# Performance work log

Hardware: AMD Instinct MI355X
Metric: run time of the kernel (lower is better)

The kernel has to match this reference:

```python
import jax, jax.numpy as jnp
import numpy as np


def setup_inputs() -> dict:
    key = jax.random.key(0)
    ks = jax.random.split(key, 8)
    B, Te, De, Dd, H = 64, 1024, 1024, 1024, 1024
    return {
        "encoder_outputs": jax.random.normal(ks[0], (B, Te, De), jnp.float32),
        "decoder_outputs": jax.random.normal(ks[1], (B, 1, Dd), jnp.float32),
        "Wa_w": jax.random.normal(ks[2], (H, Dd), jnp.float32) * 0.02,
        "Wa_b": jax.random.normal(ks[3], (H,), jnp.float32) * 0.02,
        "Ua_w": jax.random.normal(ks[4], (H, De), jnp.float32) * 0.02,
        "Ua_b": jax.random.normal(ks[5], (H,), jnp.float32) * 0.02,
        "Va_w": jax.random.normal(ks[6], (1, H), jnp.float32) * 0.02,
        "Va_b": jax.random.normal(ks[7], (1,), jnp.float32) * 0.02,
    }


def reference(encoder_outputs, decoder_outputs, Wa_w, Wa_b, Ua_w, Ua_b, Va_w, Va_b):
    # Wa: [B,1,H], Ua: [B,Te,H]  (torch Linear: x @ W.T + b)
    Wa = jnp.einsum('bqd,hd->bqh', decoder_outputs, Wa_w) + Wa_b
    Ua = jnp.einsum('bed,hd->beh', encoder_outputs, Ua_w) + Ua_b
    # broadcast add -> tanh -> scalar score per encoder position: [B,Te,1]
    scores = jnp.einsum('beh,oh->beo', jnp.tanh(Wa + Ua), Va_w) + Va_b
    scores = jnp.transpose(scores, (0, 2, 1))          # [B,1,Te]
    weights = jax.nn.softmax(scores, axis=-1)          # softmax over Te
    context = jnp.einsum('bqe,bed->bqd', weights, encoder_outputs)  # [B,1,De]
    return context
```

## Files before the change

kernel.cpp:

```cpp
#include <hip/hip_runtime.h>
#include <hip/hip_bf16.h>

#define B_  64
#define TE  1024
#define K_  1024
#define HH  1024
#define MM  (B_ * TE)

typedef __bf16 bf16x8 __attribute__((ext_vector_type(8)));
typedef __bf16 bf16x4 __attribute__((ext_vector_type(4)));
typedef float  f32x4  __attribute__((ext_vector_type(4)));

__device__ __forceinline__ float fast_tanh(float x) {
    float ax = __builtin_fabsf(x);
    float t  = __expf(-2.0f * ax);
    float r  = (1.0f - t) * __builtin_amdgcn_rcpf(1.0f + t);
    return __builtin_copysignf(r, x);
}

__global__ void zero_kernel(float* __restrict__ a, float* __restrict__ b, int n) {
    int i = blockIdx.x * blockDim.x + threadIdx.x;
    if (i < n) { a[i] = 0.0f; b[i] = 0.0f; }
}

__global__ void cvt_kernel(const float* __restrict__ in, __bf16* __restrict__ out, long n4) {
    long i = (long)blockIdx.x * blockDim.x + threadIdx.x;
    long stride = (long)gridDim.x * blockDim.x;
    const float4* in4 = (const float4*)in;
    bf16x4* out4 = (bf16x4*)out;
    for (long j = i; j < n4; j += stride) {
        float4 v = in4[j];
        bf16x4 o;
        o[0] = (__bf16)v.x; o[1] = (__bf16)v.y; o[2] = (__bf16)v.z; o[3] = (__bf16)v.w;
        out4[j] = o;
    }
}

__global__ void wa_kernel(const float* __restrict__ dec, const float* __restrict__ Wa_w,
                          const float* __restrict__ Wa_b, float* __restrict__ WaOut) {
    int b = blockIdx.x, ht = blockIdx.y;
    int wave = threadIdx.x >> 6, lane = threadIdx.x & 63;
    const float* db = dec + b * 1024;
    for (int i = 0; i < 16; i++) {
        int h = ht * 64 + wave * 16 + i;
        const float* wr = Wa_w + (long)h * 1024;
        float a = 0.0f;
        #pragma unroll
        for (int k = 0; k < 16; k++)
            a += db[lane + 64 * k] * wr[lane + 64 * k];
        #pragma unroll
        for (int off = 32; off > 0; off >>= 1)
            a += __shfl_xor(a, off, 64);
        if (lane == 0) WaOut[b * 1024 + h] = a + Wa_b[h];
    }
}

#define MT 128
#define KT 64
#define NTILES 4

__global__ __launch_bounds__(256, 4) void score_gemm(
    const __bf16* __restrict__ A,
    const __bf16* __restrict__ Bm,
    const float* __restrict__ Wa,
    const float* __restrict__ Ua_b,
    const float* __restrict__ Va_w,
    float* __restrict__ scores)
{
    __shared__ __bf16 sA[MT * KT];
    __shared__ __bf16 sB[MT * KT];
    __shared__ float sVa[512];
    __shared__ float sWU[512];

    const int tid  = threadIdx.x;
    const int wave = tid >> 6;
    const int lane = tid & 63;
    const int quad = lane >> 4;
    const int l16  = lane & 15;
    const int wm   = wave >> 1;
    const int wn   = wave & 1;

    const int rowBase = blockIdx.x * MT;
    const int colBase = blockIdx.y * (NTILES * 128);
    const int b       = rowBase >> 10;

    for (int i = tid; i < 512; i += 256) {
        int h = colBase + i;
        sVa[i] = Va_w[h];
        sWU[i] = Wa[b * 1024 + h] + Ua_b[h];
    }

    float rs[4][4] = {};

    const long aBase = (long)rowBase * K_;
    for (int nt = 0; nt < NTILES; nt++) {
        f32x4 acc[4][4] = {};
        const long bBase = (long)(colBase + nt * 128) * K_;

        for (int k0 = 0; k0 < K_; k0 += KT) {
            __syncthreads();
            #pragma unroll
            for (int i = 0; i < 4; i++) {
                int c = i * 256 + tid;
                int r = c >> 3, slot = c & 7;
                int seg = slot ^ (r & 7);
                __builtin_amdgcn_global_load_lds(
                    (const __attribute__((address_space(1))) unsigned int*)(A + aBase + (long)r * K_ + k0 + seg * 8),
                    (__attribute__((address_space(3))) unsigned int*)(sA + c * 8), 16, 0, 0);
            }
            #pragma unroll
            for (int i = 0; i < 4; i++) {
                int c = i * 256 + tid;
                int r = c >> 3, slot = c & 7;
                int seg = slot ^ (r & 7);
                __builtin_amdgcn_global_load_lds(
                    (const __attribute__((address_space(1))) unsigned int*)(Bm + bBase + (long)r * K_ + k0 + seg * 8),
                    (__attribute__((address_space(3))) unsigned int*)(sB + c * 8), 16, 0, 0);
            }
            __syncthreads();

            #pragma unroll
            for (int ks = 0; ks < 2; ks++) {
                bf16x8 bfr[4];
                #pragma unroll
                for (int t = 0; t < 4; t++) {
                    int r = wn * 64 + t * 16 + l16;
                    int slot = (ks * 4 + quad) ^ (r & 7);
                    bfr[t] = *(const bf16x8*)(sB + r * KT + slot * 8);
                }
                #pragma unroll
                for (int s = 0; s < 4; s++) {
                    int r = wm * 64 + s * 16 + l16;
                    int slot = (ks * 4 + quad) ^ (r & 7);
                    bf16x8 af = *(const bf16x8*)(sA + r * KT + slot * 8);
                    #pragma unroll
                    for (int t = 0; t < 4; t++)
                        acc[s][t] = __builtin_amdgcn_mfma_f32_16x16x32_bf16(af, bfr[t], acc[s][t], 0, 0, 0);
                }
            }
        }

        #pragma unroll
        for (int s = 0; s < 4; s++)
            #pragma unroll
            for (int t = 0; t < 4; t++) {
                int hl = nt * 128 + wn * 64 + t * 16 + l16;
                float va = sVa[hl], wu = sWU[hl];
                #pragma unroll
                for (int r = 0; r < 4; r++)
                    rs[s][r] += va * fast_tanh(acc[s][t][r] + wu);
            }
    }

    #pragma unroll
    for (int s = 0; s < 4; s++)
        #pragma unroll
        for (int r = 0; r < 4; r++) {
            float v = rs[s][r];
            v += __shfl_xor(v, 1, 64);
            v += __shfl_xor(v, 2, 64);
            v += __shfl_xor(v, 4, 64);
            v += __shfl_xor(v, 8, 64);
            if (l16 == 0)
                atomicAdd(&scores[rowBase + wm * 64 + s * 16 + quad * 4 + r], v);
        }
}

__global__ void softmax_kernel(float* __restrict__ s) {
    __shared__ float red[256];
    int b = blockIdx.x, tid = threadIdx.x;
    float4* row = (float4*)(s + b * 1024);
    float4 v = row[tid];
    float m = fmaxf(fmaxf(v.x, v.y), fmaxf(v.z, v.w));
    red[tid] = m; __syncthreads();
    for (int off = 128; off > 0; off >>= 1) {
        if (tid < off) red[tid] = fmaxf(red[tid], red[tid + off]);
        __syncthreads();
    }
    m = red[0]; __syncthreads();
    v.x = expf(v.x - m); v.y = expf(v.y - m); v.z = expf(v.z - m); v.w = expf(v.w - m);
    red[tid] = v.x + v.y + v.z + v.w; __syncthreads();
    for (int off = 128; off > 0; off >>= 1) {
        if (tid < off) red[tid] += red[tid + off];
        __syncthreads();
    }
    float inv = 1.0f / red[0];
    v.x *= inv; v.y *= inv; v.z *= inv; v.w *= inv;
    row[tid] = v;
}

__global__ void context_kernel(const __bf16* __restrict__ enc, const float* __restrict__ w,
                               float* __restrict__ out) {
    int b = blockIdx.x, ec = blockIdx.y, tid = threadIdx.x;
    const bf16x4* enc4 = (const bf16x4*)(enc + ((long)b * 1024 + ec * 64) * 1024);
    const float* wrow = w + b * 1024 + ec * 64;
    float ax = 0, ay = 0, az = 0, aw = 0;
    for (int e = 0; e < 64; e++) {
        float we = wrow[e];
        bf16x4 v = enc4[e * 256 + tid];
        ax += we * (float)v[0]; ay += we * (float)v[1];
        az += we * (float)v[2]; aw += we * (float)v[3];
    }
    float* o = out + b * 1024 + tid * 4;
    atomicAdd(o + 0, ax); atomicAdd(o + 1, ay);
    atomicAdd(o + 2, az); atomicAdd(o + 3, aw);
}

extern "C" void kernel_launch(void* const* d_in, const int* in_sizes, int n_in,
                              void* d_out, int out_size, void* d_ws, size_t ws_size,
                              hipStream_t stream) {
    (void)in_sizes; (void)n_in; (void)out_size; (void)ws_size;
    const float* enc   = (const float*)d_in[0];
    const float* dec   = (const float*)d_in[1];
    const float* Wa_w  = (const float*)d_in[2];
    const float* Wa_b  = (const float*)d_in[3];
    const float* Ua_w  = (const float*)d_in[4];
    const float* Ua_b  = (const float*)d_in[5];
    const float* Va_w  = (const float*)d_in[6];
    float* out = (float*)d_out;

    char* w = (char*)d_ws;
    __bf16* encB = (__bf16*)w;  w += (size_t)MM * 1024 * 2;
    __bf16* uawB = (__bf16*)w;  w += (size_t)HH * 1024 * 2;
    float* WaBuf = (float*)w;   w += (size_t)B_ * HH * 4;
    float* scores = (float*)w;  w += (size_t)MM * 4;

    zero_kernel<<<dim3(256), 256, 0, stream>>>(scores, out, MM);
    cvt_kernel<<<dim3(4096), 256, 0, stream>>>(enc, encB, (long)MM * 1024 / 4);
    cvt_kernel<<<dim3(256), 256, 0, stream>>>(Ua_w, uawB, (long)HH * 1024 / 4);
    wa_kernel<<<dim3(B_, 16), 256, 0, stream>>>(dec, Wa_w, Wa_b, WaBuf);
    score_gemm<<<dim3(MM / MT, HH / (NTILES * 128)), 256, 0, stream>>>(encB, uawB, WaBuf, Ua_b, Va_w, scores);
    softmax_kernel<<<dim3(B_), 256, 0, stream>>>(scores);
    context_kernel<<<dim3(B_, 16), 256, 0, stream>>>(encB, scores, out);
}
```

Before: 607.1 us.

## Widen score GEMM tile to 128x256 with grouped block swizzle

Each score_gemm block used to loop over four 128-wide H tiles and reload its A tile for every one of them. It now computes a single 128x256 output tile with 32 MFMA accumulators per wave, cutting A-tile reloads. The block index is remapped so groups of 8 row tiles share the same H columns, aiming for better L2 reuse. The zero kernel is replaced by two hipMemsetAsync calls. In exchange, register pressure rises and the launch bound drops to 2 blocks per CU. The output memset assumes out_size counts elements.

```diff
diff --git a/kernel.cpp b/kernel.cpp
--- a/kernel.cpp
+++ b/kernel.cpp
@@ -16,11 +16,6 @@
     float t  = __expf(-2.0f * ax);
     float r  = (1.0f - t) * __builtin_amdgcn_rcpf(1.0f + t);
     return __builtin_copysignf(r, x);
-}
-
-__global__ void zero_kernel(float* __restrict__ a, float* __restrict__ b, int n) {
-    int i = blockIdx.x * blockDim.x + threadIdx.x;
-    if (i < n) { a[i] = 0.0f; b[i] = 0.0f; }
 }
 
 __global__ void cvt_kernel(const float* __restrict__ in, __bf16* __restrict__ out, long n4) {
@@ -56,10 +51,10 @@
 }
 
 #define MT 128
+#define NP 256
 #define KT 64
-#define NTILES 4
-
-__global__ __launch_bounds__(256, 4) void score_gemm(
+
+__global__ __launch_bounds__(256, 2) void score_gemm(
     const __bf16* __restrict__ A,
     const __bf16* __restrict__ Bm,
     const float* __restrict__ Wa,
@@ -68,9 +63,9 @@
     float* __restrict__ scores)
 {
     __shared__ __bf16 sA[MT * KT];
-    __shared__ __bf16 sB[MT * KT];
-    __shared__ float sVa[512];
-    __shared__ float sWU[512];
+    __shared__ __bf16 sB[NP * KT];
+    __shared__ float sVa[NP];
+    __shared__ float sWU[NP];
 
     const int tid  = threadIdx.x;
     const int wave = tid >> 6;
@@ -80,77 +75,81 @@
     const int wm   = wave >> 1;
     const int wn   = wave & 1;
 
-    const int rowBase = blockIdx.x * MT;
-    const int colBase = blockIdx.y * (NTILES * 128);
+    const int bid = blockIdx.x;
+    const int grp = bid >> 5;
+    const int r5  = bid & 31;
+    const int y   = r5 >> 3;
+    const int x   = grp * 8 + (r5 & 7);
+
+    const int rowBase = x * MT;
+    const int colBase = y * NP;
     const int b       = rowBase >> 10;
 
-    for (int i = tid; i < 512; i += 256) {
-        int h = colBase + i;
-        sVa[i] = Va_w[h];
-        sWU[i] = Wa[b * 1024 + h] + Ua_b[h];
-    }
-
-    float rs[4][4] = {};
+    if (tid < NP) {
+        int h = colBase + tid;
+        sVa[tid] = Va_w[h];
+        sWU[tid] = Wa[b * 1024 + h] + Ua_b[h];
+    }
+
+    f32x4 acc[4][8] = {};
 
     const long aBase = (long)rowBase * K_;
-    for (int nt = 0; nt < NTILES; nt++) {
-        f32x4 acc[4][4] = {};
-        const long bBase = (long)(colBase + nt * 128) * K_;
-
-        for (int k0 = 0; k0 < K_; k0 += KT) {
-            __syncthreads();
+    const long bBase = (long)colBase * K_;
+
+    for (int k0 = 0; k0 < K_; k0 += KT) {
+        __syncthreads();
+        #pragma unroll
+        for (int i = 0; i < 4; i++) {
+            int c = i * 256 + tid;
+            int r = c >> 3, slot = c & 7;
+            int seg = slot ^ (r & 7);
+            __builtin_amdgcn_global_load_lds(
+                (const __attribute__((address_space(1))) unsigned int*)(A + aBase + (long)r * K_ + k0 + seg * 8),
+                (__attribute__((address_space(3))) unsigned int*)(sA + c * 8), 16, 0, 0);
+        }
+        #pragma unroll
+        for (int i = 0; i < 8; i++) {
+            int c = i * 256 + tid;
+            int r = c >> 3, slot = c & 7;
+            int seg = slot ^ (r & 7);
+            __builtin_amdgcn_global_load_lds(
+                (const __attribute__((address_space(1))) unsigned int*)(Bm + bBase + (long)r * K_ + k0 + seg * 8),
+                (__attribute__((address_space(3))) unsigned int*)(sB + c * 8), 16, 0, 0);
+        }
+        __syncthreads();
+
+        #pragma unroll
+        for (int ks = 0; ks < 2; ks++) {
+            bf16x8 bfr[8];
             #pragma unroll
-            for (int i = 0; i < 4; i++) {
-                int c = i * 256 + tid;
-                int r = c >> 3, slot = c & 7;
-                int seg = slot ^ (r & 7);
-                __builtin_amdgcn_global_load_lds(
-                    (const __attribute__((address_space(1))) unsigned int*)(A + aBase + (long)r * K_ + k0 + seg * 8),
-                    (__attribute__((address_space(3))) unsigned int*)(sA + c * 8), 16, 0, 0);
+            for (int t = 0; t < 8; t++) {
+                int r = wn * 128 + t * 16 + l16;
+                int slot = (ks * 4 + quad) ^ (r & 7);
+                bfr[t] = *(const bf16x8*)(sB + r * KT + slot * 8);
             }
             #pragma unroll
-            for (int i = 0; i < 4; i++) {
-                int c = i * 256 + tid;
-                int r = c >> 3, slot = c & 7;
-                int seg = slot ^ (r & 7);
-                __builtin_amdgcn_global_load_lds(
-                    (const __attribute__((address_space(1))) unsigned int*)(Bm + bBase + (long)r * K_ + k0 + seg * 8),
-                    (__attribute__((address_space(3))) unsigned int*)(sB + c * 8), 16, 0, 0);
+            for (int s = 0; s < 4; s++) {
+                int r = wm * 64 + s * 16 + l16;
+                int slot = (ks * 4 + quad) ^ (r & 7);
+                bf16x8 af = *(const bf16x8*)(sA + r * KT + slot * 8);
+                #pragma unroll
+                for (int t = 0; t < 8; t++)
+                    acc[s][t] = __builtin_amdgcn_mfma_f32_16x16x32_bf16(af, bfr[t], acc[s][t], 0, 0, 0);
             }
-            __syncthreads();
-
+        }
+    }
+
+    float rs[4][4] = {};
+    #pragma unroll
+    for (int s = 0; s < 4; s++)
+        #pragma unroll
+        for (int t = 0; t < 8; t++) {
+            int hl = wn * 128 + t * 16 + l16;
+            float va = sVa[hl], wu = sWU[hl];
             #pragma unroll
-            for (int ks = 0; ks < 2; ks++) {
-                bf16x8 bfr[4];
-                #pragma unroll
-                for (int t = 0; t < 4; t++) {
-                    int r = wn * 64 + t * 16 + l16;
-                    int slot = (ks * 4 + quad) ^ (r & 7);
-                    bfr[t] = *(const bf16x8*)(sB + r * KT + slot * 8);
-                }
-                #pragma unroll
-                for (int s = 0; s < 4; s++) {
-                    int r = wm * 64 + s * 16 + l16;
-                    int slot = (ks * 4 + quad) ^ (r & 7);
-                    bf16x8 af = *(const bf16x8*)(sA + r * KT + slot * 8);
-                    #pragma unroll
-                    for (int t = 0; t < 4; t++)
-                        acc[s][t] = __builtin_amdgcn_mfma_f32_16x16x32_bf16(af, bfr[t], acc[s][t], 0, 0, 0);
-                }
-            }
-        }
-
-        #pragma unroll
-        for (int s = 0; s < 4; s++)
-            #pragma unroll
-            for (int t = 0; t < 4; t++) {
-                int hl = nt * 128 + wn * 64 + t * 16 + l16;
-                float va = sVa[hl], wu = sWU[hl];
-                #pragma unroll
-                for (int r = 0; r < 4; r++)
-                    rs[s][r] += va * fast_tanh(acc[s][t][r] + wu);
-            }
-    }
+            for (int r = 0; r < 4; r++)
+                rs[s][r] += va * fast_tanh(acc[s][t][r] + wu);
+        }
 
     #pragma unroll
     for (int s = 0; s < 4; s++)
@@ -209,7 +208,7 @@
 extern "C" void kernel_launch(void* const* d_in, const int* in_sizes, int n_in,
                               void* d_out, int out_size, void* d_ws, size_t ws_size,
                               hipStream_t stream) {
-    (void)in_sizes; (void)n_in; (void)out_size; (void)ws_size;
+    (void)in_sizes; (void)n_in; (void)ws_size;
     const float* enc   = (const float*)d_in[0];
     const float* dec   = (const float*)d_in[1];
     const float* Wa_w  = (const float*)d_in[2];
@@ -225,11 +224,12 @@
     float* WaBuf = (float*)w;   w += (size_t)B_ * HH * 4;
     float* scores = (float*)w;  w += (size_t)MM * 4;
 
-    zero_kernel<<<dim3(256), 256, 0, stream>>>(scores, out, MM);
+    hipMemsetAsync(scores, 0, (size_t)MM * 4, stream);
+    hipMemsetAsync(out, 0, (size_t)out_size * 4, stream);
     cvt_kernel<<<dim3(4096), 256, 0, stream>>>(enc, encB, (long)MM * 1024 / 4);
     cvt_kernel<<<dim3(256), 256, 0, stream>>>(Ua_w, uawB, (long)HH * 1024 / 4);
     wa_kernel<<<dim3(B_, 16), 256, 0, stream>>>(dec, Wa_w, Wa_b, WaBuf);
-    score_gemm<<<dim3(MM / MT, HH / (NTILES * 128)), 256, 0, stream>>>(encB, uawB, WaBuf, Ua_b, Va_w, scores);
+    score_gemm<<<dim3((MM / MT) * (HH / NP)), 256, 0, stream>>>(encB, uawB, WaBuf, Ua_b, Va_w, scores);
     softmax_kernel<<<dim3(B_), 256, 0, stream>>>(scores);
     context_kernel<<<dim3(B_, 16), 256, 0, stream>>>(encB, scores, out);
 }
```

Measured after the change: 587.9 us. -3.2%, faster.
